# Kernel tuning notes

Hardware: AMD Instinct MI355X
Metric: run time of the kernel (lower is better)

Reference implementation:

```python
import jax, jax.numpy as jnp
import numpy as np

NU = 200000   # num user nodes
NI = 200000   # num item nodes
E = 500000    # edges per relation
D = 128       # in_feats
H = 128       # h_feats
NEG_SLOPE = 0.01  # F.leaky_relu default


def _sage(x_src, x_dst, src, dst, n_dst, W_self, W_neigh, b):
    # DGL SAGEConv('mean'): fc_self(x_dst) + fc_neigh(mean of in-neighbors) + bias
    msg = x_src[src]                                   # [E, d] gather
    agg = jax.ops.segment_sum(msg, dst, num_segments=n_dst)   # [n_dst, d]
    deg = jax.ops.segment_sum(jnp.ones((src.shape[0],), x_src.dtype), dst,
                              num_segments=n_dst)      # [n_dst]
    mean = agg / jnp.maximum(deg, 1.0)[:, None]        # zero in-degree -> 0
    return x_dst @ W_self + mean @ W_neigh + b


def setup_inputs() -> dict:
    key = jax.random.key(0)
    ks = jax.random.split(key, 20)
    s = 1.0 / np.sqrt(D)
    inp = {
        'x_user': jax.random.normal(ks[0], (NU, D), jnp.float32),
        'x_item': jax.random.normal(ks[1], (NI, D), jnp.float32),
        'w1_self_uc': jax.random.normal(ks[2], (D, H), jnp.float32) * s,
        'w1_neigh_uc': jax.random.normal(ks[3], (D, H), jnp.float32) * s,
        'b1_uc': jnp.zeros((H,), jnp.float32),
        'w1_self_iu': jax.random.normal(ks[4], (D, H), jnp.float32) * s,
        'w1_neigh_iu': jax.random.normal(ks[5], (D, H), jnp.float32) * s,
        'b1_iu': jnp.zeros((H,), jnp.float32),
        'w2_self_uc': jax.random.normal(ks[6], (H, H), jnp.float32) * s,
        'w2_neigh_uc': jax.random.normal(ks[7], (H, H), jnp.float32) * s,
        'b2_uc': jnp.zeros((H,), jnp.float32),
        'w2_self_iu': jax.random.normal(ks[8], (H, H), jnp.float32) * s,
        'w2_neigh_iu': jax.random.normal(ks[9], (H, H), jnp.float32) * s,
        'b2_iu': jnp.zeros((H,), jnp.float32),
        'src_uc': jax.random.randint(ks[10], (E,), 0, NU, jnp.int32),
        'dst_uc': jax.random.randint(ks[11], (E,), 0, NI, jnp.int32),
        'src_iu': jax.random.randint(ks[12], (E,), 0, NI, jnp.int32),
        'dst_iu': jax.random.randint(ks[13], (E,), 0, NU, jnp.int32),
    }
    return inp


def reference(x_user, x_item,
              w1_self_uc, w1_neigh_uc, b1_uc, w1_self_iu, w1_neigh_iu, b1_iu,
              w2_self_uc, w2_neigh_uc, b2_uc, w2_self_iu, w2_neigh_iu, b2_iu,
              src_uc, dst_uc, src_iu, dst_iu):
    # layer 1: relation 'clicks' user->item, relation 'clicked_by' item->user
    h1_item = _sage(x_user, x_item, src_uc, dst_uc, NI, w1_self_uc, w1_neigh_uc, b1_uc)
    h1_user = _sage(x_item, x_user, src_iu, dst_iu, NU, w1_self_iu, w1_neigh_iu, b1_iu)
    h1_item = jax.nn.leaky_relu(h1_item, NEG_SLOPE)
    h1_user = jax.nn.leaky_relu(h1_user, NEG_SLOPE)
    # layer 2
    h2_item = _sage(h1_user, h1_item, src_uc, dst_uc, NI, w2_self_uc, w2_neigh_uc, b2_uc)
    h2_user = _sage(h1_item, h1_user, src_iu, dst_iu, NU, w2_self_iu, w2_neigh_iu, b2_iu)
    # stack [user, item] (same shape) for a single output tensor
    return jnp.stack([h2_user, h2_item], axis=0)  # [2, 200000, 128]
```

## Files before the change

### kernel.cpp

```cpp
#include <hip/hip_runtime.h>
#include <hip/hip_bf16.h>

#define D_ 128

typedef __attribute__((ext_vector_type(8))) short s8b;
typedef __attribute__((ext_vector_type(4))) float f4;

union U4 { uint u[4]; s8b v; uint4 q; };

__device__ __forceinline__ void gl16(const void* g, void* lds) {
    __builtin_amdgcn_global_load_lds(
        (const __attribute__((address_space(1))) void*)g,
        (__attribute__((address_space(3))) void*)lds, 16, 0, 0);
}

__device__ __forceinline__ void split2(float f0, float f1, uint& hp, uint& lp) {
    uint u0 = __float_as_uint(f0), u1 = __float_as_uint(f1);
    hp = (u0 >> 16) | (u1 & 0xffff0000u);
    float r0 = f0 - __uint_as_float(u0 & 0xffff0000u);
    float r1 = f1 - __uint_as_float(u1 & 0xffff0000u);
    uint v0 = __float_as_uint(r0), v1 = __float_as_uint(r1);
    uint l0 = (v0 + 0x7fffu + ((v0 >> 16) & 1u)) >> 16;
    uint l1 = (v1 + 0x7fffu + ((v1 >> 16) & 1u)) >> 16;
    lp = l0 | (l1 << 16);
}

__global__ void deg2_kernel(const int* __restrict__ dstA, const int* __restrict__ dstB,
                            int* __restrict__ degA, int* __restrict__ degB, int E) {
    int e = blockIdx.x * blockDim.x + threadIdx.x;
    const int* dst = blockIdx.y ? dstB : dstA;
    int* deg = blockIdx.y ? degB : degA;
    if (e < E) atomicAdd(&deg[dst[e]], 1);
}

__global__ __launch_bounds__(256)
void scan1m(const int* __restrict__ degA, const int* __restrict__ degB,
            int* __restrict__ rpA, int* __restrict__ rpB,
            int* __restrict__ partA, int* __restrict__ partB, int N) {
    const int* deg = blockIdx.y ? degB : degA;
    int* rp = blockIdx.y ? rpB : rpA;
    int* partials = blockIdx.y ? partB : partA;
    int tid = threadIdx.x;
    int i = blockIdx.x * 256 + tid;
    int v = (i < N) ? deg[i] : 0;
    int lane = tid & 63, wid = tid >> 6;
    int x = v;
#pragma unroll
    for (int off = 1; off < 64; off <<= 1) {
        int y = __shfl_up(x, off, 64);
        if (lane >= off) x += y;
    }
    __shared__ int wsum[5];
    if (lane == 63) wsum[wid] = x;
    __syncthreads();
    if (tid == 0) {
        int a = wsum[0], b = wsum[1], c = wsum[2], d = wsum[3];
        wsum[0] = 0; wsum[1] = a; wsum[2] = a + b; wsum[3] = a + b + c;
        wsum[4] = a + b + c + d;
    }
    __syncthreads();
    if (i < N) rp[i] = wsum[wid] + x - v;
    if (tid == 0) partials[blockIdx.x] = wsum[4];
}

__global__ __launch_bounds__(1024)
void scan2m(int* __restrict__ partA, int* __restrict__ partB, int B) {
    int* partials = blockIdx.x ? partB : partA;
    __shared__ int buf[1024];
    int t = threadIdx.x;
    int v = (t < B) ? partials[t] : 0;
    buf[t] = v;
    __syncthreads();
    for (int off = 1; off < 1024; off <<= 1) {
        int add = (t >= off) ? buf[t - off] : 0;
        __syncthreads();
        buf[t] += add;
        __syncthreads();
    }
    if (t < B) partials[t] = buf[t] - v;
}

__global__ __launch_bounds__(256)
void scan3m(int* __restrict__ rpA, int* __restrict__ rpB,
            const int* __restrict__ partA, const int* __restrict__ partB, int N, int E) {
    int* rp = blockIdx.y ? rpB : rpA;
    const int* partials = blockIdx.y ? partB : partA;
    int i = blockIdx.x * 256 + threadIdx.x;
    if (i < N) rp[i] += partials[blockIdx.x];
    if (i == 0) rp[N] = E;
}

__global__ void fill2_csr(const int* __restrict__ srcA, const int* __restrict__ dstA,
                          const int* __restrict__ rpA, int* __restrict__ curA,
                          int* __restrict__ colA, int* __restrict__ colpA,
                          const int* __restrict__ srcB, const int* __restrict__ dstB,
                          const int* __restrict__ rpB, int* __restrict__ curB,
                          int* __restrict__ colB, int* __restrict__ colpB, int E) {
    int e = blockIdx.x * blockDim.x + threadIdx.x;
    if (e >= E) return;
    const int* src = blockIdx.y ? srcB : srcA;
    const int* dst = blockIdx.y ? dstB : dstA;
    const int* rp  = blockIdx.y ? rpB : rpA;
    int* cursor = blockIdx.y ? curB : curA;
    int* col    = blockIdx.y ? colB : colA;
    int* colp   = blockIdx.y ? colpB : colpA;
    int d = dst[e];
    int s = src[e];
    int idx = atomicAdd(&cursor[d], 1);
    col[rp[d] + idx] = s;
    if (idx < 4) colp[d * 4 + idx] = s;
}

__device__ __forceinline__ void acc8hl(float* a, uint4 h4, uint4 l4, float wgt) {
    const ushort* hu = (const ushort*)&h4;
    const ushort* lu = (const ushort*)&l4;
#pragma unroll
    for (int j = 0; j < 8; ++j) {
        float v = __uint_as_float((uint)hu[j] << 16) + __uint_as_float((uint)lu[j] << 16);
        a[j] = fmaf(v, wgt, a[j]);
    }
}
__device__ __forceinline__ void acc8f(float* a, float4 u0, float4 u1, float wgt) {
    a[0] = fmaf(u0.x, wgt, a[0]); a[1] = fmaf(u0.y, wgt, a[1]);
    a[2] = fmaf(u0.z, wgt, a[2]); a[3] = fmaf(u0.w, wgt, a[3]);
    a[4] = fmaf(u1.x, wgt, a[4]); a[5] = fmaf(u1.y, wgt, a[5]);
    a[6] = fmaf(u1.z, wgt, a[6]); a[7] = fmaf(u1.w, wgt, a[7]);
}

template<int INHL>
__device__ __forceinline__ void gather_node(const char* x, const int* rp,
        const int* col, const int* colp, ushort* out, int node, int li) {
    int beg = rp[node], end = rp[node + 1];
    int dg = end - beg;
    int4 c4 = *(const int4*)(colp + (size_t)node * 4);
    int s0 = dg > 0 ? c4.x : 0;
    int s1 = dg > 1 ? c4.y : 0;
    int s2 = dg > 2 ? c4.z : 0;
    int s3 = dg > 3 ? c4.w : 0;
    float w0 = dg > 0 ? 1.f : 0.f;
    float w1 = dg > 1 ? 1.f : 0.f;
    float w2 = dg > 2 ? 1.f : 0.f;
    float w3 = dg > 3 ? 1.f : 0.f;
    float a[8];
#pragma unroll
    for (int j = 0; j < 8; ++j) a[j] = 0.f;

    if (INHL) {
        const char* p0 = x + (size_t)s0 * 512 + li * 16;
        const char* p1 = x + (size_t)s1 * 512 + li * 16;
        const char* p2 = x + (size_t)s2 * 512 + li * 16;
        const char* p3 = x + (size_t)s3 * 512 + li * 16;
        uint4 H0 = *(const uint4*)p0, L0 = *(const uint4*)(p0 + 256);
        uint4 H1 = *(const uint4*)p1, L1 = *(const uint4*)(p1 + 256);
        uint4 H2 = *(const uint4*)p2, L2 = *(const uint4*)(p2 + 256);
        uint4 H3 = *(const uint4*)p3, L3 = *(const uint4*)(p3 + 256);
        acc8hl(a, H0, L0, w0); acc8hl(a, H1, L1, w1);
        acc8hl(a, H2, L2, w2); acc8hl(a, H3, L3, w3);
    } else {
        const char* p0 = x + (size_t)s0 * 512 + li * 32;
        const char* p1 = x + (size_t)s1 * 512 + li * 32;
        const char* p2 = x + (size_t)s2 * 512 + li * 32;
        const char* p3 = x + (size_t)s3 * 512 + li * 32;
        float4 A0 = *(const float4*)p0, B0 = *(const float4*)(p0 + 16);
        float4 A1 = *(const float4*)p1, B1 = *(const float4*)(p1 + 16);
        float4 A2 = *(const float4*)p2, B2 = *(const float4*)(p2 + 16);
        float4 A3 = *(const float4*)p3, B3 = *(const float4*)(p3 + 16);
        acc8f(a, A0, B0, w0); acc8f(a, A1, B1, w1);
        acc8f(a, A2, B2, w2); acc8f(a, A3, B3, w3);
    }
    for (int e = beg + 4; e < end; ++e) {
        int s = col[e];
        if (INHL) {
            const char* p = x + (size_t)s * 512 + li * 16;
            acc8hl(a, *(const uint4*)p, *(const uint4*)(p + 256), 1.f);
        } else {
            const char* p = x + (size_t)s * 512 + li * 32;
            acc8f(a, *(const float4*)p, *(const float4*)(p + 16), 1.f);
        }
    }
    float inv = 1.f / (float)(dg > 0 ? dg : 1);
    uint h0, h1, h2, h3, l0, l1, l2, l3;
    split2(a[0] * inv, a[1] * inv, h0, l0);
    split2(a[2] * inv, a[3] * inv, h1, l1);
    split2(a[4] * inv, a[5] * inv, h2, l2);
    split2(a[6] * inv, a[7] * inv, h3, l3);
    char* ob = (char*)out + (size_t)node * 512;
    *(uint4*)(ob + li * 16) = make_uint4(h0, h1, h2, h3);
    *(uint4*)(ob + 256 + li * 16) = make_uint4(l0, l1, l2, l3);
}

template<int INHL>
__global__ __launch_bounds__(256)
void gather2k(const void* xA, const int* rpA, const int* colA, const int* colpA,
              ushort* outA, int NA,
              const void* xB, const int* rpB, const int* colB, const int* colpB,
              ushort* outB, int NB, int blocksA) {
    bool isA = (int)blockIdx.x < blocksA;
    int bid = isA ? blockIdx.x : blockIdx.x - blocksA;
    long long gid = (long long)bid * 256 + threadIdx.x;
    int node = (int)(gid >> 4);
    int li = (int)(gid & 15);
    if (isA) { if (node < NA) gather_node<INHL>((const char*)xA, rpA, colA, colpA, outA, node, li); }
    else     { if (node < NB) gather_node<INHL>((const char*)xB, rpB, colB, colpB, outB, node, li); }
}

__global__ __launch_bounds__(256)
void prep_weights(const float* __restrict__ s0, const float* __restrict__ n0,
                  const float* __restrict__ s1, const float* __restrict__ n1,
                  const float* __restrict__ s2, const float* __restrict__ n2,
                  const float* __restrict__ s3, const float* __restrict__ n3,
                  ushort* __restrict__ WTH, ushort* __restrict__ WTL) {
    int g = blockIdx.y;
    int t = blockIdx.x * 256 + threadIdx.x;
    int c = t & 127;
    int oct = t >> 7;
    const float* self  = g == 0 ? s0 : g == 1 ? s1 : g == 2 ? s2 : s3;
    const float* neigh = g == 0 ? n0 : g == 1 ? n1 : g == 2 ? n2 : n3;
    uint hd[4], ld_[4];
#pragma unroll
    for (int p = 0; p < 4; ++p) {
        uint hpair = 0, lpair = 0;
#pragma unroll
        for (int q = 0; q < 2; ++q) {
            int kv = oct * 8 + p * 2 + q;
            const float* Wsrc = kv < 128 ? self : neigh;
            float f = Wsrc[(size_t)(kv & 127) * 128 + c];
            uint u = __float_as_uint(f);
            uint h = u >> 16;
            float r = f - __uint_as_float(u & 0xffff0000u);
            uint v = __float_as_uint(r);
            uint l = (v + 0x7fffu + ((v >> 16) & 1u)) >> 16;
            hpair |= h << (16 * q);
            lpair |= l << (16 * q);
        }
        hd[p] = hpair; ld_[p] = lpair;
    }
    size_t base = ((size_t)g * 128 + c) * 256 + oct * 8;
    *(uint4*)(WTH + base) = make_uint4(hd[0], hd[1], hd[2], hd[3]);
    *(uint4*)(WTL + base) = make_uint4(ld_[0], ld_[1], ld_[2], ld_[3]);
}

template<int A1FP32, int SPLIT, int LRELU>
__device__ __forceinline__ void gemm_body(const void* A1, const void* A2,
        const ushort* WTh, const ushort* WTl, const float* bias, void* outp,
        int N, int bid, char* smem) {
    const int t = threadIdx.x;
    const int w = t >> 6, lane = t & 63;
    const int fr = lane & 15, hi = lane >> 4;
    const int mrow0 = (w & 1) * 64, ncol0 = (w >> 1) * 64;
    const int row0 = bid * 128;

    f4 acc[4][4];
    {
        float bv[4];
#pragma unroll
        for (int n = 0; n < 4; ++n) bv[n] = bias[ncol0 + n * 16 + fr];
#pragma unroll
        for (int m = 0; m < 4; ++m)
#pragma unroll
            for (int n = 0; n < 4; ++n) acc[m][n] = (f4){bv[n], bv[n], bv[n], bv[n]};
    }

    for (int ks = 0; ks < 8; ++ks) {
        if (A1FP32 && ks < 4) {
            const char* src = (const char*)A1;
#pragma unroll
            for (int it = 0; it < 4; ++it) {
                int j = it * 256 + t;
                int row = j >> 3, cs = j & 7;
                int gr = row0 + row; gr = gr < N ? gr : N - 1;
                gl16(src + (size_t)gr * 512 + ks * 128 + ((cs ^ (row & 7)) * 16),
                     smem + j * 16);
            }
        } else {
            const char* src = (ks < 4) ? (const char*)A1 : (const char*)A2;
            const int kk = ks & 3;
#pragma unroll
            for (int it = 0; it < 2; ++it) {
                int j = it * 256 + t;
                int row = j >> 2, cs = j & 3;
                int gr = row0 + row; gr = gr < N ? gr : N - 1;
                size_t so = (size_t)gr * 512 + kk * 64 + ((cs ^ (row & 3)) * 16);
                gl16(src + so, smem + j * 16);
                gl16(src + so + 256, smem + 8192 + j * 16);
            }
        }
        {
#pragma unroll
            for (int it = 0; it < 2; ++it) {
                int j = it * 256 + t;
                int col = j >> 2, cs = j & 3;
                size_t so = (size_t)col * 512 + ks * 64 + ((cs ^ (col & 3)) * 16);
                gl16((const char*)WTh + so, smem + 16384 + j * 16);
                gl16((const char*)WTl + so, smem + 24576 + j * 16);
            }
        }
        __syncthreads();

        s8b ah[4], al[4], wh[4], wl[4];
        if (A1FP32 && ks < 4) {
#pragma unroll
            for (int m = 0; m < 4; ++m) {
                int r = mrow0 + m * 16 + fr;
                f4 x0 = *(const f4*)(smem + r * 128 + (((hi * 2) ^ (r & 7)) * 16));
                f4 x1 = *(const f4*)(smem + r * 128 + (((hi * 2 + 1) ^ (r & 7)) * 16));
                U4 H, L;
                split2(x0[0], x0[1], H.u[0], L.u[0]);
                split2(x0[2], x0[3], H.u[1], L.u[1]);
                split2(x1[0], x1[1], H.u[2], L.u[2]);
                split2(x1[2], x1[3], H.u[3], L.u[3]);
                ah[m] = H.v; al[m] = L.v;
            }
        } else {
#pragma unroll
            for (int m = 0; m < 4; ++m) {
                int r = mrow0 + m * 16 + fr;
                int off = r * 64 + ((hi ^ (r & 3)) * 16);
                ah[m] = *(const s8b*)(smem + off);
                al[m] = *(const s8b*)(smem + 8192 + off);
            }
        }
#pragma unroll
        for (int n = 0; n < 4; ++n) {
            int c = ncol0 + n * 16 + fr;
            int off = c * 64 + ((hi ^ (c & 3)) * 16);
            wh[n] = *(const s8b*)(smem + 16384 + off);
            wl[n] = *(const s8b*)(smem + 24576 + off);
        }
#pragma unroll
        for (int n = 0; n < 4; ++n)
#pragma unroll
            for (int m = 0; m < 4; ++m) {
                acc[m][n] = __builtin_amdgcn_mfma_f32_16x16x32_bf16(ah[m], wh[n], acc[m][n], 0, 0, 0);
                acc[m][n] = __builtin_amdgcn_mfma_f32_16x16x32_bf16(al[m], wh[n], acc[m][n], 0, 0, 0);
                acc[m][n] = __builtin_amdgcn_mfma_f32_16x16x32_bf16(ah[m], wl[n], acc[m][n], 0, 0, 0);
            }
        __syncthreads();
    }

    float* T = (float*)smem;
#pragma unroll
    for (int pass = 0; pass < 2; ++pass) {
        __syncthreads();
        if ((w & 1) == pass) {
#pragma unroll
            for (int m = 0; m < 4; ++m)
#pragma unroll
                for (int n = 0; n < 4; ++n)
#pragma unroll
                    for (int r = 0; r < 4; ++r)
                        T[(m * 16 + hi * 4 + r) * 132 + ncol0 + n * 16 + fr] = acc[m][n][r];
        }
        __syncthreads();
        int lr = t >> 2, q = t & 3;
        int gr = row0 + pass * 64 + lr;
        if (gr < N) {
#pragma unroll
            for (int i = 0; i < 4; ++i) {
                const float* p = T + lr * 132 + q * 8 + i * 32;
                f4 x0 = *(const f4*)p;
                f4 x1 = *(const f4*)(p + 4);
                float e0 = x0[0], e1 = x0[1], e2 = x0[2], e3 = x0[3];
                float e4 = x1[0], e5 = x1[1], e6 = x1[2], e7 = x1[3];
                if (LRELU) {
                    e0 = e0 > 0.f ? e0 : 0.01f * e0;
                    e1 = e1 > 0.f ? e1 : 0.01f * e1;
                    e2 = e2 > 0.f ? e2 : 0.01f * e2;
                    e3 = e3 > 0.f ? e3 : 0.01f * e3;
                    e4 = e4 > 0.f ? e4 : 0.01f * e4;
                    e5 = e5 > 0.f ? e5 : 0.01f * e5;
                    e6 = e6 > 0.f ? e6 : 0.01f * e6;
                    e7 = e7 > 0.f ? e7 : 0.01f * e7;
                }
                if (SPLIT) {
                    uint h0, h1, h2, h3, l0, l1, l2, l3;
                    split2(e0, e1, h0, l0); split2(e2, e3, h1, l1);
                    split2(e4, e5, h2, l2); split2(e6, e7, h3, l3);
                    char* ob = (char*)outp + (size_t)gr * 512;
                    *(uint4*)(ob + i * 64 + q * 16) = make_uint4(h0, h1, h2, h3);
                    *(uint4*)(ob + 256 + i * 64 + q * 16) = make_uint4(l0, l1, l2, l3);
                } else {
                    float* ob = (float*)outp + (size_t)gr * 128;
                    *(float4*)(ob + i * 32 + q * 8) = make_float4(e0, e1, e2, e3);
                    *(float4*)(ob + i * 32 + q * 8 + 4) = make_float4(e4, e5, e6, e7);
                }
            }
        }
    }
}

template<int A1FP32, int SPLIT, int LRELU>
__global__ __launch_bounds__(256)
void gemm2k(const void* A1a, const void* A2a, const ushort* WTha, const ushort* WTla,
            const float* ba, void* outa, int Na,
            const void* A1b, const void* A2b, const ushort* WThb, const ushort* WTlb,
            const float* bb, void* outb, int Nb, int blocksA) {
    __shared__ __align__(16) char smem[33792];
    bool isA = (int)blockIdx.x < blocksA;
    int bid = isA ? blockIdx.x : blockIdx.x - blocksA;
    if (isA) gemm_body<A1FP32, SPLIT, LRELU>(A1a, A2a, WTha, WTla, ba, outa, Na, bid, smem);
    else     gemm_body<A1FP32, SPLIT, LRELU>(A1b, A2b, WThb, WTlb, bb, outb, Nb, bid, smem);
}

extern "C" void kernel_launch(void* const* d_in, const int* in_sizes, int n_in,
                              void* d_out, int out_size, void* d_ws, size_t ws_size,
                              hipStream_t stream) {
    const float* x_user     = (const float*)d_in[0];
    const float* x_item     = (const float*)d_in[1];
    const float* w1_self_uc = (const float*)d_in[2];
    const float* w1_neigh_uc= (const float*)d_in[3];
    const float* b1_uc      = (const float*)d_in[4];
    const float* w1_self_iu = (const float*)d_in[5];
    const float* w1_neigh_iu= (const float*)d_in[6];
    const float* b1_iu      = (const float*)d_in[7];
    const float* w2_self_uc = (const float*)d_in[8];
    const float* w2_neigh_uc= (const float*)d_in[9];
    const float* b2_uc      = (const float*)d_in[10];
    const float* w2_self_iu = (const float*)d_in[11];
    const float* w2_neigh_iu= (const float*)d_in[12];
    const float* b2_iu      = (const float*)d_in[13];
    const int* src_uc = (const int*)d_in[14];
    const int* dst_uc = (const int*)d_in[15];
    const int* src_iu = (const int*)d_in[16];
    const int* dst_iu = (const int*)d_in[17];

    const int NU = in_sizes[0] / D_;
    const int NI = in_sizes[1] / D_;
    const int E  = in_sizes[14];

    char* hl_user = (char*)d_out;
    char* hl_item = (char*)d_out + (size_t)NU * 512;
    float* f_user = (float*)d_out;
    float* f_item = (float*)d_out + (size_t)NU * 128;

    char* ws = (char*)d_ws;
    const size_t FEAT_BYTES = (size_t)200000 * 512;
    ushort* agg_i  = (ushort*)ws; ws += FEAT_BYTES;
    ushort* agg_u  = (ushort*)ws; ws += FEAT_BYTES;
    ushort* WTH    = (ushort*)ws; ws += (size_t)4 * 128 * 256 * sizeof(ushort);
    ushort* WTL    = (ushort*)ws; ws += (size_t)4 * 128 * 256 * sizeof(ushort);
    int* colp_uc   = (int*)ws;    ws += (size_t)200000 * 4 * sizeof(int);
    int* colp_iu   = (int*)ws;    ws += (size_t)200000 * 4 * sizeof(int);
    int* rp_uc     = (int*)ws;    ws += (size_t)(NI + 1) * sizeof(int);
    int* rp_iu     = (int*)ws;    ws += (size_t)(NU + 1) * sizeof(int);
    int* col_uc    = (int*)ws;    ws += (size_t)E * sizeof(int);
    int* col_iu    = (int*)ws;    ws += (size_t)E * sizeof(int);
    int* deg_uc    = (int*)ws;    ws += (size_t)200000 * sizeof(int);
    int* deg_iu    = (int*)ws;    ws += (size_t)200000 * sizeof(int);
    int* cur_uc    = (int*)ws;    ws += (size_t)200000 * sizeof(int);
    int* cur_iu    = (int*)ws;    ws += (size_t)200000 * sizeof(int);
    int* partA     = (int*)ws;    ws += (size_t)1024 * sizeof(int);
    int* partB     = (int*)ws;    ws += (size_t)1024 * sizeof(int);

    const int TPB = 256;
    const int eBlocks  = (E + TPB - 1) / TPB;
    const int sBlocks  = (200000 + 255) / 256;
    const int gBlocksI = (int)(((long long)NI * 16 + TPB - 1) / TPB);
    const int gBlocksU = (int)(((long long)NU * 16 + TPB - 1) / TPB);
    const int mBlocksI = (NI + 127) / 128;
    const int mBlocksU = (NU + 127) / 128;
    const size_t WSTRIDE = (size_t)128 * 256;

    hipMemsetAsync(deg_uc, 0, (size_t)4 * 200000 * sizeof(int), stream);

    prep_weights<<<dim3(16, 4), 256, 0, stream>>>(
        w1_self_uc, w1_neigh_uc, w1_self_iu, w1_neigh_iu,
        w2_self_uc, w2_neigh_uc, w2_self_iu, w2_neigh_iu, WTH, WTL);

    deg2_kernel<<<dim3(eBlocks, 2), TPB, 0, stream>>>(dst_uc, dst_iu, deg_uc, deg_iu, E);
    scan1m<<<dim3(sBlocks, 2), 256, 0, stream>>>(deg_uc, deg_iu, rp_uc, rp_iu, partA, partB, 200000);
    scan2m<<<2, 1024, 0, stream>>>(partA, partB, sBlocks);
    scan3m<<<dim3(sBlocks, 2), 256, 0, stream>>>(rp_uc, rp_iu, partA, partB, 200000, E);
    fill2_csr<<<dim3(eBlocks, 2), TPB, 0, stream>>>(src_uc, dst_uc, rp_uc, cur_uc, col_uc, colp_uc,
                                                    src_iu, dst_iu, rp_iu, cur_iu, col_iu, colp_iu, E);

    gather2k<0><<<gBlocksI + gBlocksU, TPB, 0, stream>>>(
        x_user, rp_uc, col_uc, colp_uc, agg_i, NI,
        x_item, rp_iu, col_iu, colp_iu, agg_u, NU, gBlocksI);
    gemm2k<1, 1, 1><<<mBlocksI + mBlocksU, TPB, 0, stream>>>(
        x_item, agg_i, WTH + 0 * WSTRIDE, WTL + 0 * WSTRIDE, b1_uc, hl_item, NI,
        x_user, agg_u, WTH + 1 * WSTRIDE, WTL + 1 * WSTRIDE, b1_iu, hl_user, NU,
        mBlocksI);

    gather2k<1><<<gBlocksI + gBlocksU, TPB, 0, stream>>>(
        hl_user, rp_uc, col_uc, colp_uc, agg_i, NI,
        hl_item, rp_iu, col_iu, colp_iu, agg_u, NU, gBlocksI);
    gemm2k<0, 0, 0><<<mBlocksI + mBlocksU, TPB, 0, stream>>>(
        hl_item, agg_i, WTH + 2 * WSTRIDE, WTL + 2 * WSTRIDE, b2_uc, f_item, NI,
        hl_user, agg_u, WTH + 3 * WSTRIDE, WTL + 3 * WSTRIDE, b2_iu, f_user, NU,
        mBlocksI);
}
```

Measured before the change: 627.8 us.

## Halve GEMM row tile to 64 and raise occupancy with single-pass epilogue

The fused SAGE GEMM now processes 64 rows per block instead of 128, halving per-wave accumulators (2x4 tiles) and requesting 4 blocks per CU via launch bounds. The LDS swizzle is changed to use (row>>1)&3 for the narrower layout, and the epilogue writes all accumulators in one pass with each lane storing a full row segment. The aim is more resident waves to hide global-load latency, at the cost of reloading the weight tile twice as often per row and launching twice as many blocks.

```diff
diff --git a/kernel.cpp b/kernel.cpp
--- a/kernel.cpp
+++ b/kernel.cpp
@@ -247,16 +247,16 @@
     const int t = threadIdx.x;
     const int w = t >> 6, lane = t & 63;
     const int fr = lane & 15, hi = lane >> 4;
-    const int mrow0 = (w & 1) * 64, ncol0 = (w >> 1) * 64;
-    const int row0 = bid * 128;
-
-    f4 acc[4][4];
+    const int mrow0 = (w & 1) * 32, ncol0 = (w >> 1) * 64;
+    const int row0 = bid * 64;
+
+    f4 acc[2][4];
     {
         float bv[4];
 #pragma unroll
         for (int n = 0; n < 4; ++n) bv[n] = bias[ncol0 + n * 16 + fr];
 #pragma unroll
-        for (int m = 0; m < 4; ++m)
+        for (int m = 0; m < 2; ++m)
 #pragma unroll
             for (int n = 0; n < 4; ++n) acc[m][n] = (f4){bv[n], bv[n], bv[n], bv[n]};
     }
@@ -265,7 +265,7 @@
         if (A1FP32 && ks < 4) {
             const char* src = (const char*)A1;
 #pragma unroll
-            for (int it = 0; it < 4; ++it) {
+            for (int it = 0; it < 2; ++it) {
                 int j = it * 256 + t;
                 int row = j >> 3, cs = j & 7;
                 int gr = row0 + row; gr = gr < N ? gr : N - 1;
@@ -275,14 +275,13 @@
         } else {
             const char* src = (ks < 4) ? (const char*)A1 : (const char*)A2;
             const int kk = ks & 3;
-#pragma unroll
-            for (int it = 0; it < 2; ++it) {
-                int j = it * 256 + t;
+            {
+                int j = t;
                 int row = j >> 2, cs = j & 3;
                 int gr = row0 + row; gr = gr < N ? gr : N - 1;
-                size_t so = (size_t)gr * 512 + kk * 64 + ((cs ^ (row & 3)) * 16);
+                size_t so = (size_t)gr * 512 + kk * 64 + ((cs ^ ((row >> 1) & 3)) * 16);
                 gl16(src + so, smem + j * 16);
-                gl16(src + so + 256, smem + 8192 + j * 16);
+                gl16(src + so + 256, smem + 4096 + j * 16);
             }
         }
         {
@@ -290,17 +289,17 @@
             for (int it = 0; it < 2; ++it) {
                 int j = it * 256 + t;
                 int col = j >> 2, cs = j & 3;
-                size_t so = (size_t)col * 512 + ks * 64 + ((cs ^ (col & 3)) * 16);
-                gl16((const char*)WTh + so, smem + 16384 + j * 16);
-                gl16((const char*)WTl + so, smem + 24576 + j * 16);
+                size_t so = (size_t)col * 512 + ks * 64 + ((cs ^ ((col >> 1) & 3)) * 16);
+                gl16((const char*)WTh + so, smem + 8192 + j * 16);
+                gl16((const char*)WTl + so, smem + 16384 + j * 16);
             }
         }
         __syncthreads();
 
-        s8b ah[4], al[4], wh[4], wl[4];
+        s8b ah[2], al[2], wh[4], wl[4];
         if (A1FP32 && ks < 4) {
 #pragma unroll
-            for (int m = 0; m < 4; ++m) {
+            for (int m = 0; m < 2; ++m) {
                 int r = mrow0 + m * 16 + fr;
                 f4 x0 = *(const f4*)(smem + r * 128 + (((hi * 2) ^ (r & 7)) * 16));
                 f4 x1 = *(const f4*)(smem + r * 128 + (((hi * 2 + 1) ^ (r & 7)) * 16));
@@ -313,24 +312,24 @@
             }
         } else {
 #pragma unroll
-            for (int m = 0; m < 4; ++m) {
+            for (int m = 0; m < 2; ++m) {
                 int r = mrow0 + m * 16 + fr;
-                int off = r * 64 + ((hi ^ (r & 3)) * 16);
+                int off = r * 64 + ((hi ^ ((r >> 1) & 3)) * 16);
                 ah[m] = *(const s8b*)(smem + off);
-                al[m] = *(const s8b*)(smem + 8192 + off);
+                al[m] = *(const s8b*)(smem + 4096 + off);
             }
         }
 #pragma unroll
         for (int n = 0; n < 4; ++n) {
             int c = ncol0 + n * 16 + fr;
-            int off = c * 64 + ((hi ^ (c & 3)) * 16);
-            wh[n] = *(const s8b*)(smem + 16384 + off);
-            wl[n] = *(const s8b*)(smem + 24576 + off);
+            int off = c * 64 + ((hi ^ ((c >> 1) & 3)) * 16);
+            wh[n] = *(const s8b*)(smem + 8192 + off);
+            wl[n] = *(const s8b*)(smem + 16384 + off);
         }
 #pragma unroll
         for (int n = 0; n < 4; ++n)
 #pragma unroll
-            for (int m = 0; m < 4; ++m) {
+            for (int m = 0; m < 2; ++m) {
                 acc[m][n] = __builtin_amdgcn_mfma_f32_16x16x32_bf16(ah[m], wh[n], acc[m][n], 0, 0, 0);
                 acc[m][n] = __builtin_amdgcn_mfma_f32_16x16x32_bf16(al[m], wh[n], acc[m][n], 0, 0, 0);
                 acc[m][n] = __builtin_amdgcn_mfma_f32_16x16x32_bf16(ah[m], wl[n], acc[m][n], 0, 0, 0);
@@ -340,49 +339,44 @@
 
     float* T = (float*)smem;
 #pragma unroll
-    for (int pass = 0; pass < 2; ++pass) {
-        __syncthreads();
-        if ((w & 1) == pass) {
-#pragma unroll
-            for (int m = 0; m < 4; ++m)
-#pragma unroll
-                for (int n = 0; n < 4; ++n)
-#pragma unroll
-                    for (int r = 0; r < 4; ++r)
-                        T[(m * 16 + hi * 4 + r) * 132 + ncol0 + n * 16 + fr] = acc[m][n][r];
-        }
-        __syncthreads();
-        int lr = t >> 2, q = t & 3;
-        int gr = row0 + pass * 64 + lr;
+    for (int m = 0; m < 2; ++m)
+#pragma unroll
+        for (int n = 0; n < 4; ++n)
+#pragma unroll
+            for (int r = 0; r < 4; ++r)
+                T[(mrow0 + m * 16 + hi * 4 + r) * 132 + ncol0 + n * 16 + fr] = acc[m][n][r];
+    __syncthreads();
+    {
+        int gr = row0 + lane;
         if (gr < N) {
-#pragma unroll
-            for (int i = 0; i < 4; ++i) {
-                const float* p = T + lr * 132 + q * 8 + i * 32;
-                f4 x0 = *(const f4*)p;
-                f4 x1 = *(const f4*)(p + 4);
-                float e0 = x0[0], e1 = x0[1], e2 = x0[2], e3 = x0[3];
-                float e4 = x1[0], e5 = x1[1], e6 = x1[2], e7 = x1[3];
+            const float* p = T + lane * 132 + w * 32;
+#pragma unroll
+            for (int half = 0; half < 2; ++half) {
+                f4 x0 = *(const f4*)(p + half * 16);
+                f4 x1 = *(const f4*)(p + half * 16 + 4);
+                f4 x2 = *(const f4*)(p + half * 16 + 8);
+                f4 x3 = *(const f4*)(p + half * 16 + 12);
+                float e[16] = {x0[0], x0[1], x0[2], x0[3], x1[0], x1[1], x1[2], x1[3],
+                               x2[0], x2[1], x2[2], x2[3], x3[0], x3[1], x3[2], x3[3]};
                 if (LRELU) {
-                    e0 = e0 > 0.f ? e0 : 0.01f * e0;
-                    e1 = e1 > 0.f ? e1 : 0.01f * e1;
-                    e2 = e2 > 0.f ? e2 : 0.01f * e2;
-                    e3 = e3 > 0.f ? e3 : 0.01f * e3;
-                    e4 = e4 > 0.f ? e4 : 0.01f * e4;
-                    e5 = e5 > 0.f ? e5 : 0.01f * e5;
-                    e6 = e6 > 0.f ? e6 : 0.01f * e6;
-                    e7 = e7 > 0.f ? e7 : 0.01f * e7;
+#pragma unroll
+                    for (int i = 0; i < 16; ++i) e[i] = e[i] > 0.f ? e[i] : 0.01f * e[i];
                 }
                 if (SPLIT) {
-                    uint h0, h1, h2, h3, l0, l1, l2, l3;
-                    split2(e0, e1, h0, l0); split2(e2, e3, h1, l1);
-                    split2(e4, e5, h2, l2); split2(e6, e7, h3, l3);
-                    char* ob = (char*)outp + (size_t)gr * 512;
-                    *(uint4*)(ob + i * 64 + q * 16) = make_uint4(h0, h1, h2, h3);
-                    *(uint4*)(ob + 256 + i * 64 + q * 16) = make_uint4(l0, l1, l2, l3);
+                    uint h[8], l[8];
+#pragma unroll
+                    for (int i = 0; i < 8; ++i) split2(e[2 * i], e[2 * i + 1], h[i], l[i]);
+                    char* ob = (char*)outp + (size_t)gr * 512 + w * 64 + half * 32;
+                    *(uint4*)ob = make_uint4(h[0], h[1], h[2], h[3]);
+                    *(uint4*)(ob + 16) = make_uint4(h[4], h[5], h[6], h[7]);
+                    *(uint4*)(ob + 256) = make_uint4(l[0], l[1], l[2], l[3]);
+                    *(uint4*)(ob + 272) = make_uint4(l[4], l[5], l[6], l[7]);
                 } else {
-                    float* ob = (float*)outp + (size_t)gr * 128;
-                    *(float4*)(ob + i * 32 + q * 8) = make_float4(e0, e1, e2, e3);
-                    *(float4*)(ob + i * 32 + q * 8 + 4) = make_float4(e4, e5, e6, e7);
+                    float* ob = (float*)outp + (size_t)gr * 128 + w * 32 + half * 16;
+#pragma unroll
+                    for (int i = 0; i < 4; ++i)
+                        *(float4*)(ob + i * 4) = make_float4(e[i * 4], e[i * 4 + 1],
+                                                             e[i * 4 + 2], e[i * 4 + 3]);
                 }
             }
         }
@@ -390,7 +384,7 @@
 }
 
 template<int A1FP32, int SPLIT, int LRELU>
-__global__ __launch_bounds__(256)
+__global__ __launch_bounds__(256, 4)
 void gemm2k(const void* A1a, const void* A2a, const ushort* WTha, const ushort* WTla,
             const float* ba, void* outa, int Na,
             const void* A1b, const void* A2b, const ushort* WThb, const ushort* WTlb,
@@ -457,8 +451,8 @@
     const int sBlocks  = (200000 + 255) / 256;
     const int gBlocksI = (int)(((long long)NI * 16 + TPB - 1) / TPB);
     const int gBlocksU = (int)(((long long)NU * 16 + TPB - 1) / TPB);
-    const int mBlocksI = (NI + 127) / 128;
-    const int mBlocksU = (NU + 127) / 128;
+    const int mBlocksI = (NI + 63) / 64;
+    const int mBlocksU = (NU + 63) / 64;
     const size_t WSTRIDE = (size_t)128 * 256;
 
     hipMemsetAsync(deg_uc, 0, (size_t)4 * 200000 * sizeof(int), stream);
```

After: 660.1 us. +5.1%, slower.
